# Optimization experiments

Measured on AMD Instinct MI355X. Metric: run time of the kernel, lower is better.

Reference implementation:

```python
import jax, jax.numpy as jnp
import numpy as np

B, T, S, F, D, M = 8, 8192, 8192, 64, 64, 128
EPS = 1e-9


def _draw_omega(n_omega, d_feature, rng):
    # Stacked orthogonal blocks scaled by sqrt(d_feature), as in the TF module.
    n_blocks = (n_omega + d_feature - 1) // d_feature + 1
    blocks = []
    for _ in range(n_blocks):
        g = rng.standard_normal((d_feature, d_feature)).astype(np.float32)
        q, _ = np.linalg.qr(g)
        blocks.append(q * np.sqrt(float(d_feature)))
    return jnp.asarray(np.concatenate(blocks, axis=0)[:n_omega])


def setup_inputs() -> dict:
    k0 = jax.random.key(0)
    kq, kv, kk = jax.random.split(k0, 3)
    query = jax.random.normal(kq, (B, T, F), dtype=jnp.float32)
    value = jax.random.normal(kv, (B, S, D), dtype=jnp.float32)
    key = jax.random.normal(kk, (B, S, F), dtype=jnp.float32)
    omega = _draw_omega(M, F, np.random.default_rng(0))  # (M, F)
    return {"query": query, "value": value, "key": key, "omega": omega}


def _phi(x, omega):
    # x: (B, L, F) -> (B, L, 2M) positive random features
    m = omega.shape[0]
    square_sum = jnp.sum(x * x, axis=-1, keepdims=True) / 2.0  # (B, L, 1)
    xw = jnp.einsum('blf,mf->blm', x, omega)                   # (B, L, M)
    unnorm = jnp.exp(jnp.concatenate([xw, -xw], axis=-1) - square_sum) + EPS
    return unnorm / jnp.sqrt(2.0 * m)


def reference(query, value, key, omega):
    q = _phi(query, omega)  # (B, T, 2M)
    k = _phi(key, omega)    # (B, S, 2M)
    ones = jnp.ones(value.shape[:-1] + (1,), dtype=value.dtype)
    v1 = jnp.concatenate([value, ones], axis=-1)               # (B, S, D+1)
    kv = jnp.einsum('bsm,bsd->bmd', k, v1)                     # (B, 2M, D+1)
    qkv = jnp.einsum('btm,bmd->btd', q, kv)                    # (B, T, D+1)
    normalizer = qkv[:, :, -1:]
    return qkv[:, :, :-1] / normalizer
```

## Files before the change

kernel.cpp:

```cpp
#include <hip/hip_runtime.h>


constexpr int NB = 8;
constexpr int NT = 8192;
constexpr float EPSF = 1e-9f;
constexpr float SCALE = 0.0625f;

typedef short s8v __attribute__((ext_vector_type(8)));
typedef short s4v __attribute__((ext_vector_type(4)));
typedef float f4v __attribute__((ext_vector_type(4)));

__device__ inline f4v mfma16(s8v a, s8v b, f4v c) {
  return __builtin_amdgcn_mfma_f32_16x16x32_bf16(a, b, c, 0, 0, 0);
}

__device__ inline short bf16_rne(float f) {
  unsigned u = __builtin_bit_cast(unsigned, f);
  u += 0x7fffu + ((u >> 16) & 1u);
  return (short)(u >> 16);
}
__device__ inline float bf16_to_f(short h) {
  unsigned u = ((unsigned)(unsigned short)h) << 16;
  return __builtin_bit_cast(float, u);
}

__global__ void setup_omega(const float* __restrict__ omega,
                            short* __restrict__ ohf, short* __restrict__ olf) {
  int i = blockIdx.x * 256 + threadIdx.x;
  if (i >= 128 * 64) return;
  int jj = i & 7;
  int lane = (i >> 3) & 63;
  int h = (i >> 9) & 1;
  int ft = i >> 10;
  int m = ft * 16 + (lane & 15);
  int f = h * 32 + (lane >> 4) * 8 + jj;
  float wv = omega[m * 64 + f];
  short hh = bf16_rne(wv);
  ohf[i] = hh;
  olf[i] = bf16_rne(wv - bf16_to_f(hh));
}

struct PhiRows {
  s8v ah0, al0, ah1, al1;
  float ssr[4];
  float ss;
};

__device__ inline void split8(f4v a, f4v b, s8v& h, s8v& l) {
  float v[8] = {a.x, a.y, a.z, a.w, b.x, b.y, b.z, b.w};
#pragma unroll
  for (int j = 0; j < 8; ++j) {
    short hh = bf16_rne(v[j]);
    h[j] = hh;
    l[j] = bf16_rne(v[j] - bf16_to_f(hh));
  }
}

__device__ inline void load_phi_rows(const float* __restrict__ xrow_base, int lane, PhiRows& P) {
  const int r = lane & 15, q = lane >> 4;
  const float* p = xrow_base + r * 64 + q * 8;
  f4v u0 = *(const f4v*)(p);
  f4v u1 = *(const f4v*)(p + 4);
  f4v u2 = *(const f4v*)(p + 32);
  f4v u3 = *(const f4v*)(p + 36);
  float ss = u0.x * u0.x + u0.y * u0.y + u0.z * u0.z + u0.w * u0.w
           + u1.x * u1.x + u1.y * u1.y + u1.z * u1.z + u1.w * u1.w
           + u2.x * u2.x + u2.y * u2.y + u2.z * u2.z + u2.w * u2.w
           + u3.x * u3.x + u3.y * u3.y + u3.z * u3.z + u3.w * u3.w;
  ss += __shfl_xor(ss, 16, 64);
  ss += __shfl_xor(ss, 32, 64);
  ss *= 0.5f;
  P.ss = ss;
#pragma unroll
  for (int reg = 0; reg < 4; ++reg) P.ssr[reg] = __shfl(ss, q * 4 + reg, 64);
  split8(u0, u1, P.ah0, P.al0);
  split8(u2, u3, P.ah1, P.al1);
}

__device__ inline f4v phi_xw_tile(const PhiRows& P, const short* __restrict__ ohf,
                                  const short* __restrict__ olf, int ft, int lane) {
  const int o0 = ft * 1024 + lane * 8;
  s8v bh0 = *(const s8v*)(ohf + o0);
  s8v bh1 = *(const s8v*)(ohf + o0 + 512);
  s8v bl0 = *(const s8v*)(olf + o0);
  s8v bl1 = *(const s8v*)(olf + o0 + 512);
  f4v c = {0.f, 0.f, 0.f, 0.f};
  c = mfma16(P.ah0, bh0, c);
  c = mfma16(P.ah1, bh1, c);
  c = mfma16(P.al0, bh0, c);
  c = mfma16(P.al1, bh1, c);
  c = mfma16(P.ah0, bl0, c);
  c = mfma16(P.ah1, bl1, c);
  return c;
}

__device__ inline f4v phi_xw_tile_T(const PhiRows& P, const short* __restrict__ ohf,
                                    const short* __restrict__ olf, int ft, int lane) {
  const int o0 = ft * 1024 + lane * 8;
  s8v ah0 = *(const s8v*)(ohf + o0);
  s8v ah1 = *(const s8v*)(ohf + o0 + 512);
  s8v al0 = *(const s8v*)(olf + o0);
  s8v al1 = *(const s8v*)(olf + o0 + 512);
  f4v c = {0.f, 0.f, 0.f, 0.f};
  c = mfma16(ah0, P.ah0, c);
  c = mfma16(ah1, P.ah1, c);
  c = mfma16(al0, P.ah0, c);
  c = mfma16(al1, P.ah1, c);
  c = mfma16(ah0, P.al0, c);
  c = mfma16(ah1, P.al1, c);
  return c;
}

constexpr int KF_P = 72;
constexpr int QF_P = 264;
constexpr int PART_P = 72;
constexpr int PART_ROWS = 128;
constexpr int PART_SZ = PART_ROWS * PART_P;
constexpr int ACC_SZ = 256 * PART_P;
constexpr int KV_GRID = 1024;

__global__ __launch_bounds__(256, 2) void kv_fused(
    const float* __restrict__ key, const float* __restrict__ value,
    const short* __restrict__ ohf, const short* __restrict__ olf,
    short* __restrict__ partial, float* __restrict__ kvacc, int use_partial) {
  __shared__ short kft[4 * 32 * KF_P];
  const int tid = threadIdx.x, lane = tid & 63, w = tid >> 6;
  const int b = blockIdx.x >> 7;
  const int rem = blockIdx.x & 127;
  const int scb = rem >> 1, mh = rem & 1;
  const int s00 = scb * 128;
  const int q = lane >> 4, r15 = lane & 15;
  short* kw = kft + w * 32 * KF_P;

  s8v vone;
#pragma unroll
  for (int jj = 0; jj < 8; ++jj) vone[jj] = (r15 == 0) ? (short)0x3F80 : (short)0;

  f4v acc[2][5];
#pragma unroll
  for (int mt = 0; mt < 2; ++mt)
#pragma unroll
    for (int n = 0; n < 5; ++n) acc[mt][n] = f4v{0.f, 0.f, 0.f, 0.f};

  for (int sc = 0; sc < 2; ++sc) {
    const int s0 = s00 + sc * 64;
#pragma unroll 2
    for (int rg = 0; rg < 4; ++rg) {
      PhiRows P;
      load_phi_rows(key + ((size_t)b * NT + s0 + rg * 16) * 64, lane, P);
#pragma unroll
      for (int tl = 0; tl < 2; ++tl) {
        f4v c = phi_xw_tile(P, ohf, olf, w * 2 + tl, lane);
        s4v pk;
#pragma unroll
        for (int reg = 0; reg < 4; ++reg) {
          float xw = c[reg];
          float arg = mh ? (-xw - P.ssr[reg]) : (xw - P.ssr[reg]);
          pk[reg] = bf16_rne((__expf(arg) + EPSF) * SCALE);
        }
        *(s4v*)(kw + (tl * 16 + r15) * KF_P + rg * 16 + q * 4) = pk;
      }
    }
    const float* vb = value + ((size_t)b * NT + s0) * 64;
#pragma unroll
    for (int ks = 0; ks < 2; ++ks) {
      s8v bf[5];
#pragma unroll
      for (int n = 0; n < 4; ++n) {
#pragma unroll
        for (int jj = 0; jj < 8; ++jj)
          bf[n][jj] = bf16_rne(vb[(ks * 32 + q * 8 + jj) * 64 + n * 16 + r15]);
      }
      bf[4] = vone;
#pragma unroll
      for (int mt = 0; mt < 2; ++mt) {
        s8v a = *(const s8v*)(kw + (mt * 16 + r15) * KF_P + ks * 32 + q * 8);
#pragma unroll
        for (int n = 0; n < 5; ++n) acc[mt][n] = mfma16(a, bf[n], acc[mt][n]);
      }
    }
  }
  if (use_partial) {
#pragma unroll
    for (int mt = 0; mt < 2; ++mt) {
#pragma unroll
      for (int n = 0; n < 4; ++n) {
#pragma unroll
        for (int reg = 0; reg < 4; ++reg)
          kw[(mt * 16 + q * 4 + reg) * KF_P + n * 16 + r15] = bf16_rne(acc[mt][n][reg]);
      }
      if (r15 == 0) {
#pragma unroll
        for (int reg = 0; reg < 4; ++reg)
          kw[(mt * 16 + q * 4 + reg) * KF_P + 64] = bf16_rne(acc[mt][4][reg]);
      }
    }
    short* pb = partial + (size_t)blockIdx.x * PART_SZ + w * 32 * PART_P;
#pragma unroll
    for (int i = 0; i < 9; ++i) {
      int e = i * 64 + lane;
      *(s4v*)(pb + e * 4) = *(const s4v*)(kw + e * 4);
    }
  } else {
    float* pb = kvacc + (size_t)b * ACC_SZ;
#pragma unroll
    for (int mt = 0; mt < 2; ++mt) {
#pragma unroll
      for (int reg = 0; reg < 4; ++reg) {
        int m = mh * 128 + w * 32 + mt * 16 + q * 4 + reg;
#pragma unroll
        for (int n = 0; n < 4; ++n)
          atomicAdd(pb + (size_t)m * PART_P + n * 16 + r15, acc[mt][n][reg]);
        if (r15 == 0) atomicAdd(pb + (size_t)m * PART_P + 64, acc[mt][4][reg]);
      }
    }
  }
}

__global__ __launch_bounds__(256) void kv_finalize(
    const short* __restrict__ partial, const float* __restrict__ kvacc,
    short* __restrict__ kvfrag, int use_partial) {
  int i = blockIdx.x * 256 + threadIdx.x;
  int b = i / 20480;
  int rem = i - b * 20480;
  int m = rem / 80;
  int d = rem - m * 80;
  float s = 0.f;
  if (d < 65) {
    if (use_partial) {
      int mh = m >> 7, pr = m & 127;
      const short* p = partial + ((size_t)(b * 128 + mh)) * PART_SZ + pr * PART_P + d;
#pragma unroll 8
      for (int c = 0; c < 64; ++c) s += bf16_to_f(p[(size_t)c * 2 * PART_SZ]);
    } else {
      s = kvacc[(size_t)b * ACC_SZ + (size_t)m * PART_P + d];
    }
  }
  int ks = m >> 5, qq = (m >> 3) & 3, j = m & 7;
  int n = d >> 4, r = d & 15;
  int lane = qq * 16 + r;
  if (d < 80)
    kvfrag[(((size_t)b * 40 + ks * 5 + n) * 64 + lane) * 8 + j] = bf16_rne(s);
}

__global__ __launch_bounds__(256, 4) void qkv_fused(
    const float* __restrict__ query, const short* __restrict__ ohf,
    const short* __restrict__ olf, const short* __restrict__ kvfrag,
    float* __restrict__ out) {
  __shared__ __align__(16) short qf[64 * QF_P];
  const int tid = threadIdx.x, lane = tid & 63, w = tid >> 6;
  const int b = blockIdx.x >> 7;
  const int t0 = (blockIdx.x & 127) * 64;
  const int q = lane >> 4, r15 = lane & 15;

  {
    PhiRows P;
    load_phi_rows(query + ((size_t)b * NT + t0 + w * 16) * 64, lane, P);
    const int t_loc = w * 16 + r15;
#pragma unroll
    for (int ft = 0; ft < 8; ++ft) {
      f4v c = phi_xw_tile_T(P, ohf, olf, ft, lane);
      s4v pk, nk;
#pragma unroll
      for (int reg = 0; reg < 4; ++reg) {
        float xw = c[reg];
        pk[reg] = bf16_rne((__expf(xw - P.ss) + EPSF) * SCALE);
        nk[reg] = bf16_rne((__expf(-xw - P.ss) + EPSF) * SCALE);
      }
      *(s4v*)(qf + t_loc * QF_P + ft * 16 + q * 4) = pk;
      *(s4v*)(qf + t_loc * QF_P + 128 + ft * 16 + q * 4) = nk;
    }
  }
  f4v acc[5];
#pragma unroll
  for (int n = 0; n < 5; ++n) acc[n] = f4v{0.f, 0.f, 0.f, 0.f};
  const short* kvb = kvfrag + (size_t)b * 40 * 512;
#pragma unroll
  for (int ks = 0; ks < 8; ++ks) {
    s8v a = *(const s8v*)(qf + (w * 16 + r15) * QF_P + ks * 32 + q * 8);
#pragma unroll
    for (int n = 0; n < 5; ++n) {
      s8v bf = *(const s8v*)(kvb + ((size_t)(ks * 5 + n)) * 512 + lane * 8);
      acc[n] = mfma16(a, bf, acc[n]);
    }
  }
  float den_r[4];
#pragma unroll
  for (int reg = 0; reg < 4; ++reg) den_r[reg] = __shfl(acc[4][reg], lane & 48, 64);
  float* stg = (float*)(qf + w * 16 * QF_P);
#pragma unroll
  for (int n = 0; n < 4; ++n)
#pragma unroll
    for (int reg = 0; reg < 4; ++reg) {
      int row = q * 4 + reg;
      int col = n * 16 + r15;
      stg[row * 68 + col] = acc[n][reg] / den_r[reg];
    }
  float* ob = out + ((size_t)b * NT + t0 + w * 16) * 64;
#pragma unroll
  for (int rr = 0; rr < 4; ++rr) {
    int row = rr * 4 + q;
    int c4 = r15 * 4;
    *(f4v*)(ob + row * 64 + c4) = *(const f4v*)(stg + row * 68 + c4);
  }
}

extern "C" void kernel_launch(void* const* d_in, const int* in_sizes, int n_in,
                              void* d_out, int out_size, void* d_ws, size_t ws_size,
                              hipStream_t stream) {
  const float* query = (const float*)d_in[0];
  const float* value = (const float*)d_in[1];
  const float* key   = (const float*)d_in[2];
  const float* omega = (const float*)d_in[3];
  float* out = (float*)d_out;

  char* ws = (char*)d_ws;
  short* ohf = (short*)ws;
  short* olf = (short*)(ws + 16384);
  short* kvfrag = (short*)(ws + 32768);
  short* partial = (short*)(ws + 360448);
  float* kvacc = (float*)(ws + 360448);
  const size_t need_full = 360448 + (size_t)KV_GRID * PART_SZ * 2;
  const int use_partial = (ws_size >= need_full) ? 1 : 0;

  setup_omega<<<32, 256, 0, stream>>>(omega, ohf, olf);
  if (!use_partial) {
    hipMemsetAsync(kvacc, 0, (size_t)8 * ACC_SZ * 4, stream);
  }
  kv_fused<<<KV_GRID, 256, 0, stream>>>(key, value, ohf, olf, partial, kvacc, use_partial);
  kv_finalize<<<640, 256, 0, stream>>>(partial, kvacc, kvfrag, use_partial);
  qkv_fused<<<1024, 256, 0, stream>>>(query, ohf, olf, kvfrag, out);
}
```

Baseline: 134.8 us.

## Compute positive and negative key features from one xw tile per block

Each kv_fused block now covers both halves of the random-feature dimension, with 512 threads across 8 waves instead of two blocks each handling one sign. Each wave computes one xw tile and produces both exp(xw) and exp(-xw) from it. This halves the key loads, the omega MFMA work and the value reloads across blocks. In exchange the blocks are larger and need more LDS, the grid shrinks to 512, and the partial-buffer layout and the finalize indexing change to match.

```diff
diff --git a/kernel.cpp b/kernel.cpp
--- a/kernel.cpp
+++ b/kernel.cpp
@@ -114,21 +114,18 @@
 constexpr int KF_P = 72;
 constexpr int QF_P = 264;
 constexpr int PART_P = 72;
-constexpr int PART_ROWS = 128;
-constexpr int PART_SZ = PART_ROWS * PART_P;
+constexpr int PART_SZ = 256 * PART_P;
 constexpr int ACC_SZ = 256 * PART_P;
-constexpr int KV_GRID = 1024;
-
-__global__ __launch_bounds__(256, 2) void kv_fused(
+constexpr int KV_GRID = 512;
+
+__global__ __launch_bounds__(512, 2) void kv_fused(
     const float* __restrict__ key, const float* __restrict__ value,
     const short* __restrict__ ohf, const short* __restrict__ olf,
     short* __restrict__ partial, float* __restrict__ kvacc, int use_partial) {
-  __shared__ short kft[4 * 32 * KF_P];
+  __shared__ short kft[8 * 32 * KF_P];
   const int tid = threadIdx.x, lane = tid & 63, w = tid >> 6;
-  const int b = blockIdx.x >> 7;
-  const int rem = blockIdx.x & 127;
-  const int scb = rem >> 1, mh = rem & 1;
-  const int s00 = scb * 128;
+  const int b = blockIdx.x >> 6;
+  const int s00 = (blockIdx.x & 63) * 128;
   const int q = lane >> 4, r15 = lane & 15;
   short* kw = kft + w * 32 * KF_P;
 
@@ -148,18 +145,16 @@
     for (int rg = 0; rg < 4; ++rg) {
       PhiRows P;
       load_phi_rows(key + ((size_t)b * NT + s0 + rg * 16) * 64, lane, P);
-#pragma unroll
-      for (int tl = 0; tl < 2; ++tl) {
-        f4v c = phi_xw_tile(P, ohf, olf, w * 2 + tl, lane);
-        s4v pk;
-#pragma unroll
-        for (int reg = 0; reg < 4; ++reg) {
-          float xw = c[reg];
-          float arg = mh ? (-xw - P.ssr[reg]) : (xw - P.ssr[reg]);
-          pk[reg] = bf16_rne((__expf(arg) + EPSF) * SCALE);
-        }
-        *(s4v*)(kw + (tl * 16 + r15) * KF_P + rg * 16 + q * 4) = pk;
-      }
+      f4v c = phi_xw_tile(P, ohf, olf, w, lane);
+      s4v pk, nk;
+#pragma unroll
+      for (int reg = 0; reg < 4; ++reg) {
+        float xw = c[reg];
+        pk[reg] = bf16_rne((__expf(xw - P.ssr[reg]) + EPSF) * SCALE);
+        nk[reg] = bf16_rne((__expf(-xw - P.ssr[reg]) + EPSF) * SCALE);
+      }
+      *(s4v*)(kw + (r15) * KF_P + rg * 16 + q * 4) = pk;
+      *(s4v*)(kw + (16 + r15) * KF_P + rg * 16 + q * 4) = nk;
     }
     const float* vb = value + ((size_t)b * NT + s0) * 64;
 #pragma unroll
@@ -207,7 +202,8 @@
     for (int mt = 0; mt < 2; ++mt) {
 #pragma unroll
       for (int reg = 0; reg < 4; ++reg) {
-        int m = mh * 128 + w * 32 + mt * 16 + q * 4 + reg;
+        int ml = q * 4 + reg;
+        int m = (mt == 0) ? (w * 16 + ml) : (128 + w * 16 + ml);
 #pragma unroll
         for (int n = 0; n < 4; ++n)
           atomicAdd(pb + (size_t)m * PART_P + n * 16 + r15, acc[mt][n][reg]);
@@ -228,10 +224,13 @@
   float s = 0.f;
   if (d < 65) {
     if (use_partial) {
-      int mh = m >> 7, pr = m & 127;
-      const short* p = partial + ((size_t)(b * 128 + mh)) * PART_SZ + pr * PART_P + d;
+      int w_, ml;
+      if (m < 128) { w_ = m >> 4; ml = m & 15; }
+      else { int mm = m - 128; w_ = mm >> 4; ml = 16 + (mm & 15); }
+      int pr = w_ * 32 + ml;
+      const short* p = partial + (size_t)(b * 64) * PART_SZ + pr * PART_P + d;
 #pragma unroll 8
-      for (int c = 0; c < 64; ++c) s += bf16_to_f(p[(size_t)c * 2 * PART_SZ]);
+      for (int c = 0; c < 64; ++c) s += bf16_to_f(p[(size_t)c * PART_SZ]);
     } else {
       s = kvacc[(size_t)b * ACC_SZ + (size_t)m * PART_P + d];
     }
@@ -327,7 +326,7 @@
   if (!use_partial) {
     hipMemsetAsync(kvacc, 0, (size_t)8 * ACC_SZ * 4, stream);
   }
-  kv_fused<<<KV_GRID, 256, 0, stream>>>(key, value, ohf, olf, partial, kvacc, use_partial);
+  kv_fused<<<KV_GRID, 512, 0, stream>>>(key, value, ohf, olf, partial, kvacc, use_partial);
   kv_finalize<<<640, 256, 0, stream>>>(partial, kvacc, kvfrag, use_partial);
   qkv_fused<<<1024, 256, 0, stream>>>(query, ohf, olf, kvfrag, out);
 }
```

Measured after the change: 131.4 us. 1.03x faster.
